# Kernel tuning notes

Measured on AMD Instinct MI355X. Metric: run time of the kernel, lower is better.

## Reference

```python
import jax, jax.numpy as jnp
import numpy as np

B = 16384; NF = 16; VOCAB = 100000; ED = 32; NNUM = 13
E = 8; T = 2; H0 = 512; H1 = 256; TH = 128
D0 = NF * ED + NNUM  # 525
EPS = 1e-5


def setup_inputs() -> dict:
    key = jax.random.key(0)
    ks = jax.random.split(key, 24)
    f32 = jnp.float32
    return {
        "categorical_x": jax.random.randint(ks[0], (B, NF), 0, VOCAB),
        "numerical_x": jax.random.normal(ks[1], (B, NNUM), f32),
        "epoch": 5,  # >= M -> MoE (not if_neuron) branch
        "emb_table": jax.random.normal(ks[2], (NF * VOCAB, ED), f32) * 0.05,
        "W0": jax.random.normal(ks[3], (E, D0, H0), f32) * 0.05,
        "b0": jnp.zeros((E, H0), f32),
        "bn0_gamma": 1.0 + 0.1 * jax.random.normal(ks[4], (H0,), f32),
        "bn0_beta": 0.1 * jax.random.normal(ks[5], (H0,), f32),
        "bn0_mean": 0.1 * jax.random.normal(ks[6], (H0,), f32),
        "bn0_var": 0.5 + jax.random.uniform(ks[7], (H0,), f32),
        "W1": jax.random.normal(ks[8], (E, H0, H1), f32) * 0.05,
        "b1": jnp.zeros((E, H1), f32),
        "bn1_gamma": 1.0 + 0.1 * jax.random.normal(ks[9], (H1,), f32),
        "bn1_beta": 0.1 * jax.random.normal(ks[10], (H1,), f32),
        "bn1_mean": 0.1 * jax.random.normal(ks[11], (H1,), f32),
        "bn1_var": 0.5 + jax.random.uniform(ks[12], (H1,), f32),
        "Wg": jax.random.normal(ks[13], (T, D0, E), f32) * 0.05,
        "bg": jnp.zeros((T, E), f32),
        "Wt1": jax.random.normal(ks[14], (T, H1, TH), f32) * 0.05,
        "bt1": jnp.zeros((T, TH), f32),
        "tbn_gamma": 1.0 + 0.1 * jax.random.normal(ks[15], (T, TH), f32),
        "tbn_beta": 0.1 * jax.random.normal(ks[16], (T, TH), f32),
        "tbn_mean": 0.1 * jax.random.normal(ks[17], (T, TH), f32),
        "tbn_var": 0.5 + jax.random.uniform(ks[18], (T, TH), f32),
        "Wt2": jax.random.normal(ks[19], (T, TH, 1), f32) * 0.05,
        "bt2": jnp.zeros((T, 1), f32),
    }


def reference(categorical_x, numerical_x, epoch, emb_table,
              W0, b0, bn0_gamma, bn0_beta, bn0_mean, bn0_var,
              W1, b1, bn1_gamma, bn1_beta, bn1_mean, bn1_var,
              Wg, bg, Wt1, bt1, tbn_gamma, tbn_beta, tbn_mean, tbn_var,
              Wt2, bt2):
    # --- embedding + concat ---
    offsets = jnp.arange(NF, dtype=categorical_x.dtype) * VOCAB
    emb = emb_table[categorical_x + offsets[None, :]].reshape(B, NF * ED)
    x = jnp.concatenate([emb, numerical_x], axis=1)  # [B, D0]

    def bn(h, g, b, m, v):  # eval-mode BatchNorm1d, params shared across experts
        return (h - m) * jax.lax.rsqrt(v + EPS) * g + b

    # --- per-expert layer 0: grouped GEMM + shared BN/ReLU (Dropout eval=id) ---
    h = jnp.einsum('bd,edk->ebk', x, W0) + b0[:, None, :]          # [E,B,H0]
    h = jax.nn.relu(bn(h, bn0_gamma, bn0_beta, bn0_mean, bn0_var))
    # --- per-expert layer 1 ---
    h = jnp.einsum('ebd,edk->ebk', h, W1) + b1[:, None, :]          # [E,B,H1]
    h = jax.nn.relu(bn(h, bn1_gamma, bn1_beta, bn1_mean, bn1_var))

    expert_output = jnp.transpose(h, (1, 0, 2))                     # [B,E,H1]
    # --- per-task softmax gates over the raw input, bmm combine ---
    gates = jax.nn.softmax(jnp.einsum('bd,tde->tbe', x, Wg) + bg[:, None, :], axis=-1)  # [T,B,E]
    fea = jnp.einsum('tbe,bek->tbk', gates, expert_output)          # [T,B,H1]

    # --- per-task tower MLP: Linear -> BN -> ReLU -> Linear, sigmoid ---
    t = jnp.einsum('tbk,tkh->tbh', fea, Wt1) + bt1[:, None, :]      # [T,B,TH]
    t = (t - tbn_mean[:, None, :]) * jax.lax.rsqrt(tbn_var[:, None, :] + EPS)
    t = jax.nn.relu(t * tbn_gamma[:, None, :] + tbn_beta[:, None, :])
    out = (jnp.einsum('tbh,tho->tbo', t, Wt2) + bt2[:, None, :])[..., 0]  # [T,B]
    return jax.nn.sigmoid(out)
```

## Files before the change

### kernel.cpp

```cpp
#include <hip/hip_runtime.h>
#include <hip/hip_bf16.h>

#define B_ 16384
#define NF_ 16
#define VOCAB_ 100000
#define ED_ 32
#define NNUM_ 13
#define E_ 8
#define T_ 2
#define H0_ 512
#define H1_ 256
#define TH_ 128
#define D0_ 525
#define K0P 576

#define BM 128
#define BN 128
#define BKK 64

typedef __bf16 bf16x8 __attribute__((ext_vector_type(8)));
typedef float  f32x4  __attribute__((ext_vector_type(4)));
typedef int    i32x4  __attribute__((ext_vector_type(4)));

typedef __attribute__((address_space(3))) void lds_void;
typedef __attribute__((address_space(1))) const void gbl_void;

__device__ __forceinline__ void load_lds16(const void* g, void* l) {
  __builtin_amdgcn_global_load_lds((gbl_void*)g, (lds_void*)l, 16, 0, 0);
}

__global__ __launch_bounds__(192) void k_embed(const int* __restrict__ cat,
                                               const float* __restrict__ num,
                                               const float* __restrict__ emb,
                                               __hip_bfloat16* __restrict__ x) {
  int b = blockIdx.x;
  int t = threadIdx.x;
  const int* crow = cat + b * NF_;
#pragma unroll
  for (int i = 0; i < 3; ++i) {
    int d = t + i * 192;
    float v;
    if (d < 512) {
      int f = d >> 5, c = d & 31;
      v = emb[((long long)(f * VOCAB_ + crow[f])) * ED_ + c];
    } else if (d < D0_) {
      v = num[b * NNUM_ + (d - 512)];
    } else {
      v = 0.f;
    }
    x[(long long)b * K0P + d] = __float2bfloat16(v);
  }
}

__global__ __launch_bounds__(256) void k_wprep(const float* __restrict__ W,
                                               __hip_bfloat16* __restrict__ Wp,
                                               int K, int N, int KP) {
  __shared__ float tile[64][65];
  int k0 = blockIdx.x * 64, n0 = blockIdx.y * 64, e = blockIdx.z;
  int tx = threadIdx.x & 63, ty = threadIdx.x >> 6;
  for (int r = ty; r < 64; r += 4) {
    int k = k0 + r;
    tile[r][tx] = (k < K) ? W[((long long)e * K + k) * N + n0 + tx] : 0.f;
  }
  __syncthreads();
  for (int r = ty; r < 64; r += 4) {
    int n = n0 + r;
    Wp[((long long)e * N + n) * KP + k0 + tx] = __float2bfloat16(tile[tx][r]);
  }
}

__global__ void k_prep_small(const float* b0, const float* g0, const float* be0,
                             const float* m0, const float* v0,
                             const float* b1, const float* g1, const float* be1,
                             const float* m1, const float* v1,
                             const float* bt1, const float* tg, const float* tb,
                             const float* tm, const float* tv,
                             float* scale0, float* ebias0, float* scale1, float* ebias1,
                             float* tscale, float* tbias) {
  int i = blockIdx.x * 256 + threadIdx.x;
  if (i < H0_) scale0[i] = g0[i] * rsqrtf(v0[i] + 1e-5f);
  if (i < H1_) scale1[i] = g1[i] * rsqrtf(v1[i] + 1e-5f);
  if (i < T_ * TH_) {
    float s = tg[i] * rsqrtf(tv[i] + 1e-5f);
    tscale[i] = s;
    tbias[i] = (bt1[i] - tm[i]) * s + tb[i];
  }
  if (i < E_ * H0_) {
    int n = i & (H0_ - 1);
    float s = g0[n] * rsqrtf(v0[n] + 1e-5f);
    ebias0[i] = (b0[i] - m0[n]) * s + be0[n];
  }
  if (i < E_ * H1_) {
    int n = i & (H1_ - 1);
    float s = g1[n] * rsqrtf(v1[n] + 1e-5f);
    ebias1[i] = (b1[i] - m1[n]) * s + be1[n];
  }
}

__global__ __launch_bounds__(256) void k_gates(const __hip_bfloat16* __restrict__ x,
                                               const float* __restrict__ Wg,
                                               const float* __restrict__ bg,
                                               float* __restrict__ gates) {
  int gidx = blockIdx.x * 256 + threadIdx.x;
  int b = gidx >> 4, te = gidx & 15;
  int t = te >> 3, e = te & 7;
  const __hip_bfloat16* xr = x + (long long)b * K0P;
  const float* wg = Wg + ((long long)t * D0_) * E_ + e;
  float acc = bg[t * E_ + e];
  int k = 0;
  for (; k + 8 <= D0_; k += 8) {
    bf16x8 xv = *reinterpret_cast<const bf16x8*>(xr + k);
#pragma unroll
    for (int j = 0; j < 8; ++j)
      acc += (float)xv[j] * wg[(long long)(k + j) * E_];
  }
  for (; k < D0_; ++k) acc += __bfloat162float(xr[k]) * wg[(long long)k * E_];
  float mx = acc;
#pragma unroll
  for (int o = 1; o < 8; o <<= 1) mx = fmaxf(mx, __shfl_xor(mx, o));
  float p = __expf(acc - mx);
  float s = p;
#pragma unroll
  for (int o = 1; o < 8; o <<= 1) s += __shfl_xor(s, o);
  gates[((long long)t * B_ + b) * E_ + e] = p / s;
}

__global__ __launch_bounds__(256) void k_gemm(
    const __hip_bfloat16* __restrict__ Aall, long long strideAe, int lda,
    const __hip_bfloat16* __restrict__ Ball, long long strideBe, int ldb,
    __hip_bfloat16* __restrict__ Call, long long strideCe, int N,
    const float* __restrict__ scale, const float* __restrict__ ebias, int strideEb,
    int K) {
  __shared__ __align__(16) char As[BM * 128];
  __shared__ __align__(16) char Bs[BN * 128];

  const int e = blockIdx.z;
  const char* A = reinterpret_cast<const char*>(Aall + (long long)e * strideAe +
                                                (long long)blockIdx.x * BM * lda);
  const char* Bw = reinterpret_cast<const char*>(Ball + (long long)e * strideBe +
                                                 (long long)blockIdx.y * BN * ldb);
  const int ldab = lda * 2, ldbb = ldb * 2;

  const int tid = threadIdx.x;
  const int lane = tid & 63;
  const int wid = tid >> 6;
  const int wr = wid >> 1, wc = wid & 1;

  const int baserow = wid * 32 + (lane >> 3);
  const int swz = ((lane & 7) << 4) ^ ((lane >> 3) << 4);

  f32x4 acc[4][4];
#pragma unroll
  for (int m = 0; m < 4; ++m)
#pragma unroll
    for (int n = 0; n < 4; ++n) acc[m][n] = (f32x4){0.f, 0.f, 0.f, 0.f};

  const int nk = K / BKK;
  for (int ks = 0; ks < nk; ++ks) {
    const int kb0 = ks * 128;
#pragma unroll
    for (int i = 0; i < 4; ++i) {
      const int row = baserow + i * 8;
      load_lds16(A + (long long)row * ldab + kb0 + swz, As + (wid * 4 + i) * 1024);
      load_lds16(Bw + (long long)row * ldbb + kb0 + swz, Bs + (wid * 4 + i) * 1024);
    }
    __syncthreads();
#pragma unroll
    for (int kk = 0; kk < 2; ++kk) {
      bf16x8 af[4], bfr[4];
      int kb = kk * 64 + (lane >> 4) * 16;
#pragma unroll
      for (int m = 0; m < 4; ++m) {
        int row = wr * 64 + m * 16 + (lane & 15);
        af[m] = *reinterpret_cast<const bf16x8*>(As + row * 128 + (kb ^ ((row & 7) << 4)));
      }
#pragma unroll
      for (int n = 0; n < 4; ++n) {
        int row = wc * 64 + n * 16 + (lane & 15);
        bfr[n] = *reinterpret_cast<const bf16x8*>(Bs + row * 128 + (kb ^ ((row & 7) << 4)));
      }
#pragma unroll
      for (int m = 0; m < 4; ++m)
#pragma unroll
        for (int n = 0; n < 4; ++n)
          acc[m][n] = __builtin_amdgcn_mfma_f32_16x16x32_bf16(af[m], bfr[n], acc[m][n], 0, 0, 0);
    }
    __syncthreads();
  }

  __hip_bfloat16* C = Call + (long long)e * strideCe;
  const float* eb = ebias + e * strideEb;
  const int m0 = blockIdx.x * BM, n0 = blockIdx.y * BN;
#pragma unroll
  for (int n = 0; n < 4; ++n) {
    int col = n0 + wc * 64 + n * 16 + (lane & 15);
    float s = scale[col];
    float bb = eb[col];
#pragma unroll
    for (int m = 0; m < 4; ++m) {
      int rowb = m0 + wr * 64 + m * 16 + (lane >> 4) * 4;
#pragma unroll
      for (int i = 0; i < 4; ++i) {
        float v = fmaxf(acc[m][n][i] * s + bb, 0.f);
        C[(long long)(rowb + i) * N + col] = __float2bfloat16(v);
      }
    }
  }
}

__global__ __launch_bounds__(256) void k_tower(
    const __hip_bfloat16* __restrict__ h1, const float* __restrict__ gates,
    const float* __restrict__ Wt1, const float* __restrict__ Wt2,
    const float* __restrict__ bt2, const float* __restrict__ tscale,
    const float* __restrict__ tbias, float* __restrict__ out) {
  __shared__ __align__(16) char Ws[TH_ * 512];
  const int tid = threadIdx.x;
  const int lane = tid & 63, wv = tid >> 6;

  const int row = blockIdx.x * 64 + wv * 16 + (lane & 15);
  const int g4 = lane >> 4;

  float gt0[8], gt1[8];
  {
    const float* gp0 = gates + (long long)row * E_;
    const float* gp1 = gates + ((long long)B_ + row) * E_;
#pragma unroll
    for (int j = 0; j < 8; ++j) { gt0[j] = gp0[j]; gt1[j] = gp1[j]; }
  }

  float fa0[8][8], fa1[8][8];
#pragma unroll
  for (int c = 0; c < 8; ++c)
#pragma unroll
    for (int j = 0; j < 8; ++j) { fa0[c][j] = 0.f; fa1[c][j] = 0.f; }

#pragma unroll
  for (int ee = 0; ee < 8; ++ee) {
    const char* hp = reinterpret_cast<const char*>(h1) +
                     (((long long)ee * B_ + row) * H1_ + g4 * 8) * 2;
    float ga = gt0[ee], gb = gt1[ee];
#pragma unroll
    for (int c = 0; c < 8; ++c) {
      bf16x8 hv = *reinterpret_cast<const bf16x8*>(hp + c * 64);
#pragma unroll
      for (int j = 0; j < 8; ++j) {
        float v = (float)hv[j];
        fa0[c][j] += ga * v;
        fa1[c][j] += gb * v;
      }
    }
  }
  bf16x8 af0[8], af1[8];
#pragma unroll
  for (int c = 0; c < 8; ++c)
#pragma unroll
    for (int j = 0; j < 8; ++j) {
      af0[c][j] = (__bf16)fa0[c][j];
      af1[c][j] = (__bf16)fa1[c][j];
    }

#pragma unroll
  for (int t = 0; t < T_; ++t) {
    if (t) __syncthreads();
    for (int it = 0; it < 16; ++it) {
      int idx = it * 256 + tid;
      int h = idx & 127, kc = idx >> 7;
      bf16x8 v;
#pragma unroll
      for (int j = 0; j < 8; ++j)
        v[j] = (__bf16)Wt1[((long long)t * H1_ + kc * 8 + j) * TH_ + h];
      int byt = h * 512 + ((kc * 16) ^ ((h & 7) << 4));
      *reinterpret_cast<bf16x8*>(Ws + byt) = v;
    }
    __syncthreads();

    f32x4 acc[8];
#pragma unroll
    for (int n = 0; n < 8; ++n) acc[n] = (f32x4){0.f, 0.f, 0.f, 0.f};
#pragma unroll
    for (int c = 0; c < 8; ++c) {
      int kb = c * 64 + g4 * 16;
#pragma unroll
      for (int n = 0; n < 8; ++n) {
        int hrow = n * 16 + (lane & 15);
        bf16x8 bv = *reinterpret_cast<const bf16x8*>(Ws + hrow * 512 + (kb ^ ((hrow & 7) << 4)));
        acc[n] = __builtin_amdgcn_mfma_f32_16x16x32_bf16(t ? af1[c] : af0[c], bv, acc[n], 0, 0, 0);
      }
    }

    float part[4] = {0.f, 0.f, 0.f, 0.f};
#pragma unroll
    for (int n = 0; n < 8; ++n) {
      int col = n * 16 + (lane & 15);
      float s = tscale[t * TH_ + col], bb = tbias[t * TH_ + col], w2 = Wt2[t * TH_ + col];
#pragma unroll
      for (int i = 0; i < 4; ++i)
        part[i] += fmaxf(acc[n][i] * s + bb, 0.f) * w2;
    }
#pragma unroll
    for (int o = 1; o < 16; o <<= 1) {
#pragma unroll
      for (int i = 0; i < 4; ++i) part[i] += __shfl_xor(part[i], o);
    }
    if ((lane & 15) == 0) {
      int rbase = blockIdx.x * 64 + wv * 16 + g4 * 4;
      float b2 = bt2[t];
#pragma unroll
      for (int i = 0; i < 4; ++i) {
        float z = part[i] + b2;
        out[(long long)t * B_ + rbase + i] = 1.f / (1.f + __expf(-z));
      }
    }
  }
}

extern "C" void kernel_launch(void* const* d_in, const int* in_sizes, int n_in,
                              void* d_out, int out_size, void* d_ws, size_t ws_size,
                              hipStream_t stream) {
  const int*   cat = (const int*)d_in[0];
  const float* num = (const float*)d_in[1];
  const float* emb = (const float*)d_in[3];
  const float* W0  = (const float*)d_in[4];
  const float* b0  = (const float*)d_in[5];
  const float* g0  = (const float*)d_in[6];
  const float* be0 = (const float*)d_in[7];
  const float* m0  = (const float*)d_in[8];
  const float* v0  = (const float*)d_in[9];
  const float* W1  = (const float*)d_in[10];
  const float* b1  = (const float*)d_in[11];
  const float* g1  = (const float*)d_in[12];
  const float* be1 = (const float*)d_in[13];
  const float* m1  = (const float*)d_in[14];
  const float* v1  = (const float*)d_in[15];
  const float* Wg  = (const float*)d_in[16];
  const float* bg  = (const float*)d_in[17];
  const float* Wt1 = (const float*)d_in[18];
  const float* bt1 = (const float*)d_in[19];
  const float* tg  = (const float*)d_in[20];
  const float* tb  = (const float*)d_in[21];
  const float* tm  = (const float*)d_in[22];
  const float* tv  = (const float*)d_in[23];
  const float* Wt2 = (const float*)d_in[24];
  const float* bt2 = (const float*)d_in[25];
  float* out = (float*)d_out;

  char* ws = (char*)d_ws;
  if (ws_size < 228094976ULL) return;

  __hip_bfloat16* x_bf = (__hip_bfloat16*)(ws + 0ULL);
  __hip_bfloat16* W0p  = (__hip_bfloat16*)(ws + 18874368ULL);
  __hip_bfloat16* W1p  = (__hip_bfloat16*)(ws + 23592960ULL);
  float* gates   = (float*)(ws + 25690112ULL);
  float* scale0  = (float*)(ws + 26738688ULL);
  float* ebias0  = (float*)(ws + 26740736ULL);
  float* scale1  = (float*)(ws + 26757120ULL);
  float* ebias1  = (float*)(ws + 26758144ULL);
  float* tscale  = (float*)(ws + 26766336ULL);
  float* tbias   = (float*)(ws + 26767360ULL);
  __hip_bfloat16* h0 = (__hip_bfloat16*)(ws + 26768384ULL);
  __hip_bfloat16* h1 = (__hip_bfloat16*)(ws + 160986112ULL);

  k_wprep<<<dim3(K0P / 64, H0_ / 64, E_), 256, 0, stream>>>(W0, W0p, D0_, H0_, K0P);
  k_wprep<<<dim3(H0_ / 64, H1_ / 64, E_), 256, 0, stream>>>(W1, W1p, H0_, H1_, H0_);
  k_prep_small<<<16, 256, 0, stream>>>(b0, g0, be0, m0, v0, b1, g1, be1, m1, v1,
                                       bt1, tg, tb, tm, tv,
                                       scale0, ebias0, scale1, ebias1, tscale, tbias);
  k_embed<<<B_, 192, 0, stream>>>(cat, num, emb, x_bf);
  k_gates<<<B_ * 16 / 256, 256, 0, stream>>>(x_bf, Wg, bg, gates);
  k_gemm<<<dim3(B_ / BM, H0_ / BN, E_), 256, 0, stream>>>(
      x_bf, 0LL, K0P, W0p, (long long)H0_ * K0P, K0P,
      h0, (long long)B_ * H0_, H0_, scale0, ebias0, H0_, K0P);
  k_gemm<<<dim3(B_ / BM, H1_ / BN, E_), 256, 0, stream>>>(
      h0, (long long)B_ * H0_, H0_, W1p, (long long)H1_ * H0_, H0_,
      h1, (long long)B_ * H1_, H1_, scale1, ebias1, H1_, H0_);
  k_tower<<<dim3(B_ / 64), 256, 0, stream>>>(h1, gates, Wt1, Wt2, bt2,
                                             tscale, tbias, out);
}
```

Baseline: 312.9 us.

## Enlarge GEMM tiles to 256x256 with double-buffered LDS prefetch

The grouped expert GEMM moves from 128x128 tiles with 256 threads to 256x256 tiles with 512 threads (8 waves, each computing 128x64). The LDS staging is double-buffered so the next K tile's global-to-LDS loads are issued before computing the current one, with explicit vmcnt waits and raw barriers. It also raises MFMA wave priority with s_setprio. The larger tiles raise data reuse and cut global traffic, but they use 128KB of LDS and 128 accumulator registers per thread. This may limit occupancy and leaves fewer blocks for the second GEMM (N=256 gives one column tile).

```diff
diff --git a/kernel.cpp b/kernel.cpp
--- a/kernel.cpp
+++ b/kernel.cpp
@@ -14,9 +14,8 @@
 #define D0_ 525
 #define K0P 576
 
-#define BM 128
-#define BN 128
-#define BKK 64
+#define GBM 256
+#define GBN 256
 
 typedef __bf16 bf16x8 __attribute__((ext_vector_type(8)));
 typedef float  f32x4  __attribute__((ext_vector_type(4)));
@@ -25,7 +24,7 @@
 typedef __attribute__((address_space(3))) void lds_void;
 typedef __attribute__((address_space(1))) const void gbl_void;
 
-__device__ __forceinline__ void load_lds16(const void* g, void* l) {
+__device__ __forceinline__ void load_lds16f(const void* g, void* l) {
   __builtin_amdgcn_global_load_lds((gbl_void*)g, (lds_void*)l, 16, 0, 0);
 }
 
@@ -125,80 +124,113 @@
   gates[((long long)t * B_ + b) * E_ + e] = p / s;
 }
 
-__global__ __launch_bounds__(256) void k_gemm(
+__global__ __launch_bounds__(512, 2) void k_gemm(
     const __hip_bfloat16* __restrict__ Aall, long long strideAe, int lda,
     const __hip_bfloat16* __restrict__ Ball, long long strideBe, int ldb,
     __hip_bfloat16* __restrict__ Call, long long strideCe, int N,
     const float* __restrict__ scale, const float* __restrict__ ebias, int strideEb,
     int K) {
-  __shared__ __align__(16) char As[BM * 128];
-  __shared__ __align__(16) char Bs[BN * 128];
+  __shared__ __align__(16) char As[2][32768];
+  __shared__ __align__(16) char Bs[2][32768];
 
   const int e = blockIdx.z;
   const char* A = reinterpret_cast<const char*>(Aall + (long long)e * strideAe +
-                                                (long long)blockIdx.x * BM * lda);
+                                                (long long)blockIdx.x * GBM * lda);
   const char* Bw = reinterpret_cast<const char*>(Ball + (long long)e * strideBe +
-                                                 (long long)blockIdx.y * BN * ldb);
+                                                 (long long)blockIdx.y * GBN * ldb);
   const int ldab = lda * 2, ldbb = ldb * 2;
 
   const int tid = threadIdx.x;
   const int lane = tid & 63;
   const int wid = tid >> 6;
-  const int wr = wid >> 1, wc = wid & 1;
-
-  const int baserow = wid * 32 + (lane >> 3);
-  const int swz = ((lane & 7) << 4) ^ ((lane >> 3) << 4);
-
-  f32x4 acc[4][4];
-#pragma unroll
-  for (int m = 0; m < 4; ++m)
+  const int wr = wid >> 2, wc = wid & 3;
+
+  const int stg_row = tid >> 3;
+  const int swz = ((tid & 7) << 4) ^ ((stg_row & 7) << 4);
+
+  f32x4 acc[8][4];
+#pragma unroll
+  for (int m = 0; m < 8; ++m)
 #pragma unroll
     for (int n = 0; n < 4; ++n) acc[m][n] = (f32x4){0.f, 0.f, 0.f, 0.f};
 
-  const int nk = K / BKK;
-  for (int ks = 0; ks < nk; ++ks) {
-    const int kb0 = ks * 128;
-#pragma unroll
-    for (int i = 0; i < 4; ++i) {
-      const int row = baserow + i * 8;
-      load_lds16(A + (long long)row * ldab + kb0 + swz, As + (wid * 4 + i) * 1024);
-      load_lds16(Bw + (long long)row * ldbb + kb0 + swz, Bs + (wid * 4 + i) * 1024);
-    }
-    __syncthreads();
-#pragma unroll
-    for (int kk = 0; kk < 2; ++kk) {
-      bf16x8 af[4], bfr[4];
-      int kb = kk * 64 + (lane >> 4) * 16;
-#pragma unroll
-      for (int m = 0; m < 4; ++m) {
-        int row = wr * 64 + m * 16 + (lane & 15);
-        af[m] = *reinterpret_cast<const bf16x8*>(As + row * 128 + (kb ^ ((row & 7) << 4)));
+  const int nk = K / 64;
+
+#define STAGE_TILE(kt_, s_)                                                     \
+  do {                                                                          \
+    const long long kb0_ = (long long)(kt_) * 128;                              \
+    char* adst_ = As[(s_)] + tid * 16;                                          \
+    char* bdst_ = Bs[(s_)] + tid * 16;                                          \
+    _Pragma("unroll")                                                           \
+    for (int i_ = 0; i_ < 4; ++i_) {                                            \
+      const int row_ = stg_row + i_ * 64;                                       \
+      load_lds16f(A + (long long)row_ * ldab + kb0_ + swz, adst_ + i_ * 8192);  \
+      load_lds16f(Bw + (long long)row_ * ldbb + kb0_ + swz, bdst_ + i_ * 8192); \
+    }                                                                           \
+  } while (0)
+
+  STAGE_TILE(0, 0);
+
+  for (int kt = 0; kt < nk; ++kt) {
+    const int cur = kt & 1;
+    if (kt + 1 < nk) {
+      STAGE_TILE(kt + 1, cur ^ 1);
+      asm volatile("s_waitcnt vmcnt(8)" ::: "memory");
+    } else {
+      asm volatile("s_waitcnt vmcnt(0)" ::: "memory");
+    }
+    __builtin_amdgcn_s_barrier();
+
+    const char* Ab = As[cur];
+    const char* Bb = Bs[cur];
+#pragma unroll
+    for (int mh = 0; mh < 2; ++mh)
+#pragma unroll
+      for (int nh = 0; nh < 2; ++nh) {
+        bf16x8 af[2][4], bq[2][2];
+#pragma unroll
+        for (int kk = 0; kk < 2; ++kk) {
+          const int kb = kk * 64 + (lane >> 4) * 16;
+#pragma unroll
+          for (int m = 0; m < 4; ++m) {
+            const int row = wr * 128 + (mh * 4 + m) * 16 + (lane & 15);
+            af[kk][m] = *reinterpret_cast<const bf16x8*>(
+                Ab + row * 128 + (kb ^ ((row & 7) << 4)));
+          }
+#pragma unroll
+          for (int n = 0; n < 2; ++n) {
+            const int row = wc * 64 + (nh * 2 + n) * 16 + (lane & 15);
+            bq[kk][n] = *reinterpret_cast<const bf16x8*>(
+                Bb + row * 128 + (kb ^ ((row & 7) << 4)));
+          }
+        }
+        __builtin_amdgcn_s_setprio(1);
+#pragma unroll
+        for (int kk = 0; kk < 2; ++kk)
+#pragma unroll
+          for (int m = 0; m < 4; ++m)
+#pragma unroll
+            for (int n = 0; n < 2; ++n)
+              acc[mh * 4 + m][nh * 2 + n] = __builtin_amdgcn_mfma_f32_16x16x32_bf16(
+                  af[kk][m], bq[kk][n], acc[mh * 4 + m][nh * 2 + n], 0, 0, 0);
+        __builtin_amdgcn_s_setprio(0);
       }
-#pragma unroll
-      for (int n = 0; n < 4; ++n) {
-        int row = wc * 64 + n * 16 + (lane & 15);
-        bfr[n] = *reinterpret_cast<const bf16x8*>(Bs + row * 128 + (kb ^ ((row & 7) << 4)));
-      }
-#pragma unroll
-      for (int m = 0; m < 4; ++m)
-#pragma unroll
-        for (int n = 0; n < 4; ++n)
-          acc[m][n] = __builtin_amdgcn_mfma_f32_16x16x32_bf16(af[m], bfr[n], acc[m][n], 0, 0, 0);
-    }
-    __syncthreads();
-  }
+    asm volatile("" ::: "memory");
+    __builtin_amdgcn_s_barrier();
+  }
+#undef STAGE_TILE
 
   __hip_bfloat16* C = Call + (long long)e * strideCe;
   const float* eb = ebias + e * strideEb;
-  const int m0 = blockIdx.x * BM, n0 = blockIdx.y * BN;
+  const int m0 = blockIdx.x * GBM, n0 = blockIdx.y * GBN;
 #pragma unroll
   for (int n = 0; n < 4; ++n) {
     int col = n0 + wc * 64 + n * 16 + (lane & 15);
     float s = scale[col];
     float bb = eb[col];
 #pragma unroll
-    for (int m = 0; m < 4; ++m) {
-      int rowb = m0 + wr * 64 + m * 16 + (lane >> 4) * 4;
+    for (int m = 0; m < 8; ++m) {
+      int rowb = m0 + wr * 128 + m * 16 + (lane >> 4) * 4;
 #pragma unroll
       for (int i = 0; i < 4; ++i) {
         float v = fmaxf(acc[m][n][i] * s + bb, 0.f);
@@ -367,10 +399,10 @@
                                        scale0, ebias0, scale1, ebias1, tscale, tbias);
   k_embed<<<B_, 192, 0, stream>>>(cat, num, emb, x_bf);
   k_gates<<<B_ * 16 / 256, 256, 0, stream>>>(x_bf, Wg, bg, gates);
-  k_gemm<<<dim3(B_ / BM, H0_ / BN, E_), 256, 0, stream>>>(
+  k_gemm<<<dim3(B_ / GBM, H0_ / GBN, E_), 512, 0, stream>>>(
       x_bf, 0LL, K0P, W0p, (long long)H0_ * K0P, K0P,
       h0, (long long)B_ * H0_, H0_, scale0, ebias0, H0_, K0P);
-  k_gemm<<<dim3(B_ / BM, H1_ / BN, E_), 256, 0, stream>>>(
+  k_gemm<<<dim3(B_ / GBM, H1_ / GBN, E_), 512, 0, stream>>>(
       h0, (long long)B_ * H0_, H0_, W1p, (long long)H1_ * H0_, H0_,
       h1, (long long)B_ * H1_, H1_, scale1, ebias1, H1_, H0_);
   k_tower<<<dim3(B_ / 64), 256, 0, stream>>>(h1, gates, Wt1, Wt2, bt2,
```

New measurement: 318.4 us. Within noise of the previous version (+1.7%).

## Rewrite expert GEMM as 256x256 double-buffered ping-pong pipeline with 8 waves

Applied to the files above, without the earlier changes.

Replaces the 128x128 single-buffered GEMM with a 256x256 tile per 512-thread block. Each operand is split into halves and double-buffered in LDS, and async global-to-LDS loads are interleaved with quadrant MFMA phases behind explicit barriers and setprio. The K padding is raised from 576 to 640 so the K loop runs an even number of 64-wide steps, which adds some zero-padded work in layer 0. The aim is to hide load latency and raise arithmetic intensity, at the cost of 128KB of LDS per block, more registers and lower occupancy.

```diff
diff --git a/kernel.cpp b/kernel.cpp
--- a/kernel.cpp
+++ b/kernel.cpp
@@ -12,24 +12,32 @@
 #define H1_ 256
 #define TH_ 128
 #define D0_ 525
-#define K0P 576
-
-#define BM 128
-#define BN 128
-#define BKK 64
+#define K0P 640
 
 typedef __bf16 bf16x8 __attribute__((ext_vector_type(8)));
 typedef float  f32x4  __attribute__((ext_vector_type(4)));
-typedef int    i32x4  __attribute__((ext_vector_type(4)));
 
 typedef __attribute__((address_space(3))) void lds_void;
 typedef __attribute__((address_space(1))) const void gbl_void;
 
-__device__ __forceinline__ void load_lds16(const void* g, void* l) {
+__device__ __forceinline__ void load_lds16f(const void* g, void* l) {
   __builtin_amdgcn_global_load_lds((gbl_void*)g, (lds_void*)l, 16, 0, 0);
 }
 
-__global__ __launch_bounds__(192) void k_embed(const int* __restrict__ cat,
+#define BARX                                        \
+  do {                                              \
+    asm volatile("" ::: "memory");                  \
+    __builtin_amdgcn_s_barrier();                   \
+    __builtin_amdgcn_sched_barrier(0);              \
+    asm volatile("" ::: "memory");                  \
+  } while (0)
+#define LGKM0                                       \
+  do {                                              \
+    asm volatile("s_waitcnt lgkmcnt(0)" ::: "memory"); \
+    __builtin_amdgcn_sched_barrier(0);              \
+  } while (0)
+
+__global__ __launch_bounds__(256) void k_embed(const int* __restrict__ cat,
                                                const float* __restrict__ num,
                                                const float* __restrict__ emb,
                                                __hip_bfloat16* __restrict__ x) {
@@ -38,7 +46,8 @@
   const int* crow = cat + b * NF_;
 #pragma unroll
   for (int i = 0; i < 3; ++i) {
-    int d = t + i * 192;
+    int d = t + i * 256;
+    if (d >= K0P) continue;
     float v;
     if (d < 512) {
       int f = d >> 5, c = d & 31;
@@ -125,87 +134,159 @@
   gates[((long long)t * B_ + b) * E_ + e] = p / s;
 }
 
-__global__ __launch_bounds__(256) void k_gemm(
+__global__ __launch_bounds__(512, 2) void k_gemm(
     const __hip_bfloat16* __restrict__ Aall, long long strideAe, int lda,
     const __hip_bfloat16* __restrict__ Ball, long long strideBe, int ldb,
     __hip_bfloat16* __restrict__ Call, long long strideCe, int N,
     const float* __restrict__ scale, const float* __restrict__ ebias, int strideEb,
     int K) {
-  __shared__ __align__(16) char As[BM * 128];
-  __shared__ __align__(16) char Bs[BN * 128];
+  __shared__ __align__(16) char As[2][2][16384];
+  __shared__ __align__(16) char Bs[2][2][16384];
 
   const int e = blockIdx.z;
   const char* A = reinterpret_cast<const char*>(Aall + (long long)e * strideAe +
-                                                (long long)blockIdx.x * BM * lda);
+                                                (long long)blockIdx.x * 256 * lda);
   const char* Bw = reinterpret_cast<const char*>(Ball + (long long)e * strideBe +
-                                                 (long long)blockIdx.y * BN * ldb);
+                                                 (long long)blockIdx.y * 256 * ldb);
   const int ldab = lda * 2, ldbb = ldb * 2;
 
   const int tid = threadIdx.x;
   const int lane = tid & 63;
   const int wid = tid >> 6;
-  const int wr = wid >> 1, wc = wid & 1;
-
-  const int baserow = wid * 32 + (lane >> 3);
-  const int swz = ((lane & 7) << 4) ^ ((lane >> 3) << 4);
-
-  f32x4 acc[4][4];
-#pragma unroll
-  for (int m = 0; m < 4; ++m)
-#pragma unroll
-    for (int n = 0; n < 4; ++n) acc[m][n] = (f32x4){0.f, 0.f, 0.f, 0.f};
-
-  const int nk = K / BKK;
-  for (int ks = 0; ks < nk; ++ks) {
-    const int kb0 = ks * 128;
-#pragma unroll
-    for (int i = 0; i < 4; ++i) {
-      const int row = baserow + i * 8;
-      load_lds16(A + (long long)row * ldab + kb0 + swz, As + (wid * 4 + i) * 1024);
-      load_lds16(Bw + (long long)row * ldbb + kb0 + swz, Bs + (wid * 4 + i) * 1024);
-    }
-    __syncthreads();
+  const int wq_r = wid >> 2, wq_c = wid & 3;
+
+  const int srow = tid >> 3;
+  const int swz = ((tid & 7) << 4) ^ ((srow & 7) << 4);
+
+  auto STG_A = [&](int kt, int half, int slot) {
+#pragma unroll
+    for (int j = 0; j < 2; ++j) {
+      const int lrow = srow + j * 64;
+      load_lds16f(A + (long long)(half * 128 + lrow) * ldab + kt * 128 + swz,
+                  &As[slot][half][j * 8192 + tid * 16]);
+    }
+  };
+  auto STG_B = [&](int kt, int half, int slot) {
+#pragma unroll
+    for (int j = 0; j < 2; ++j) {
+      const int lrow = srow + j * 64;
+      load_lds16f(Bw + (long long)(half * 128 + lrow) * ldbb + kt * 128 + swz,
+                  &Bs[slot][half][j * 8192 + tid * 16]);
+    }
+  };
+
+  bf16x8 af[2][4], bq[2][2];
+  auto LDA = [&](int slot, int half) {
 #pragma unroll
     for (int kk = 0; kk < 2; ++kk) {
-      bf16x8 af[4], bfr[4];
-      int kb = kk * 64 + (lane >> 4) * 16;
+      const int kb = kk * 64 + (lane >> 4) * 16;
 #pragma unroll
       for (int m = 0; m < 4; ++m) {
-        int row = wr * 64 + m * 16 + (lane & 15);
-        af[m] = *reinterpret_cast<const bf16x8*>(As + row * 128 + (kb ^ ((row & 7) << 4)));
-      }
-#pragma unroll
-      for (int n = 0; n < 4; ++n) {
-        int row = wc * 64 + n * 16 + (lane & 15);
-        bfr[n] = *reinterpret_cast<const bf16x8*>(Bs + row * 128 + (kb ^ ((row & 7) << 4)));
-      }
+        const int lrow = wq_r * 64 + m * 16 + (lane & 15);
+        af[kk][m] = *reinterpret_cast<const bf16x8*>(
+            &As[slot][half][lrow * 128 + (kb ^ ((lane & 7) << 4))]);
+      }
+    }
+  };
+  auto LDB = [&](int slot, int half) {
+#pragma unroll
+    for (int kk = 0; kk < 2; ++kk) {
+      const int kb = kk * 64 + (lane >> 4) * 16;
+#pragma unroll
+      for (int n = 0; n < 2; ++n) {
+        const int lrow = wq_c * 32 + n * 16 + (lane & 15);
+        bq[kk][n] = *reinterpret_cast<const bf16x8*>(
+            &Bs[slot][half][lrow * 128 + (kb ^ ((lane & 7) << 4))]);
+      }
+    }
+  };
+
+  f32x4 acc[2][2][4][2];
+#pragma unroll
+  for (int a = 0; a < 2; ++a)
+#pragma unroll
+    for (int b = 0; b < 2; ++b)
 #pragma unroll
       for (int m = 0; m < 4; ++m)
 #pragma unroll
-        for (int n = 0; n < 4; ++n)
-          acc[m][n] = __builtin_amdgcn_mfma_f32_16x16x32_bf16(af[m], bfr[n], acc[m][n], 0, 0, 0);
-    }
-    __syncthreads();
-  }
+        for (int n = 0; n < 2; ++n) acc[a][b][m][n] = (f32x4){0.f, 0.f, 0.f, 0.f};
+
+#define MMQ(QM, QN)                                                            \
+  do {                                                                         \
+    __builtin_amdgcn_s_setprio(1);                                             \
+    _Pragma("unroll") for (int kk = 0; kk < 2; ++kk)                           \
+        _Pragma("unroll") for (int m = 0; m < 4; ++m)                          \
+            _Pragma("unroll") for (int n = 0; n < 2; ++n)                      \
+                acc[QM][QN][m][n] = __builtin_amdgcn_mfma_f32_16x16x32_bf16(   \
+                    af[kk][m], bq[kk][n], acc[QM][QN][m][n], 0, 0, 0);         \
+    __builtin_amdgcn_s_setprio(0);                                             \
+  } while (0)
+
+  const int nk = K / 64;
+  const int nj = nk / 2;
+
+  STG_A(0, 0, 0); STG_A(0, 1, 0); STG_B(0, 0, 0); STG_B(0, 1, 0);
+  if (nk > 1) { STG_A(1, 0, 1); STG_B(1, 1, 1); }
+  asm volatile("s_waitcnt vmcnt(4)" ::: "memory");
+  BARX;
+
+  for (int j = 0; j < nj; ++j) {
+    const int t1 = 2 * j + 1, t2 = 2 * j + 2, t3 = 2 * j + 3;
+    const bool more = (t2 < nk);
+    LDA(0, 0); LDB(0, 0);
+    STG_A(t1, 1, 1);
+    BARX; LGKM0; MMQ(0, 0); BARX;
+    LDB(0, 1);
+    STG_B(t1, 0, 1);
+    BARX; LGKM0; MMQ(0, 1); BARX;
+    LDA(0, 1);
+    if (more) STG_A(t2, 0, 0);
+    BARX; LGKM0; MMQ(1, 1); BARX;
+    LDB(0, 0);
+    if (more) STG_B(t2, 1, 0);
+    BARX; LGKM0; MMQ(1, 0);
+    if (more) { asm volatile("s_waitcnt vmcnt(4)" ::: "memory"); }
+    else      { asm volatile("s_waitcnt vmcnt(0)" ::: "memory"); }
+    BARX;
+    LDA(1, 0); LDB(1, 0);
+    if (more) STG_A(t2, 1, 0);
+    BARX; LGKM0; MMQ(0, 0); BARX;
+    LDB(1, 1);
+    if (more) STG_B(t2, 0, 0);
+    BARX; LGKM0; MMQ(0, 1); BARX;
+    LDA(1, 1);
+    if (more) STG_A(t3, 0, 1);
+    BARX; LGKM0; MMQ(1, 1); BARX;
+    LDB(1, 0);
+    if (more) STG_B(t3, 1, 1);
+    BARX; LGKM0; MMQ(1, 0);
+    if (more) { asm volatile("s_waitcnt vmcnt(4)" ::: "memory"); }
+    BARX;
+  }
+#undef MMQ
 
   __hip_bfloat16* C = Call + (long long)e * strideCe;
   const float* eb = ebias + e * strideEb;
-  const int m0 = blockIdx.x * BM, n0 = blockIdx.y * BN;
-#pragma unroll
-  for (int n = 0; n < 4; ++n) {
-    int col = n0 + wc * 64 + n * 16 + (lane & 15);
-    float s = scale[col];
-    float bb = eb[col];
-#pragma unroll
-    for (int m = 0; m < 4; ++m) {
-      int rowb = m0 + wr * 64 + m * 16 + (lane >> 4) * 4;
-#pragma unroll
-      for (int i = 0; i < 4; ++i) {
-        float v = fmaxf(acc[m][n][i] * s + bb, 0.f);
-        C[(long long)(rowb + i) * N + col] = __float2bfloat16(v);
-      }
-    }
-  }
+  const int m0 = blockIdx.x * 256, n0 = blockIdx.y * 256;
+#pragma unroll
+  for (int Qm = 0; Qm < 2; ++Qm)
+#pragma unroll
+    for (int Qn = 0; Qn < 2; ++Qn)
+#pragma unroll
+      for (int n = 0; n < 2; ++n) {
+        const int col = n0 + Qn * 128 + wq_c * 32 + n * 16 + (lane & 15);
+        const float s = scale[col];
+        const float bb = eb[col];
+#pragma unroll
+        for (int m = 0; m < 4; ++m) {
+          const int rowb = m0 + Qm * 128 + wq_r * 64 + m * 16 + (lane >> 4) * 4;
+#pragma unroll
+          for (int i = 0; i < 4; ++i) {
+            float v = fmaxf(acc[Qm][Qn][m][n][i] * s + bb, 0.f);
+            C[(long long)(rowb + i) * N + col] = __float2bfloat16(v);
+          }
+        }
+      }
 }
 
 __global__ __launch_bounds__(256) void k_tower(
@@ -345,32 +426,32 @@
   float* out = (float*)d_out;
 
   char* ws = (char*)d_ws;
-  if (ws_size < 228094976ULL) return;
+  if (ws_size < 230719488ULL) return;
 
   __hip_bfloat16* x_bf = (__hip_bfloat16*)(ws + 0ULL);
-  __hip_bfloat16* W0p  = (__hip_bfloat16*)(ws + 18874368ULL);
-  __hip_bfloat16* W1p  = (__hip_bfloat16*)(ws + 23592960ULL);
-  float* gates   = (float*)(ws + 25690112ULL);
-  float* scale0  = (float*)(ws + 26738688ULL);
-  float* ebias0  = (float*)(ws + 26740736ULL);
-  float* scale1  = (float*)(ws + 26757120ULL);
-  float* ebias1  = (float*)(ws + 26758144ULL);
-  float* tscale  = (float*)(ws + 26766336ULL);
-  float* tbias   = (float*)(ws + 26767360ULL);
-  __hip_bfloat16* h0 = (__hip_bfloat16*)(ws + 26768384ULL);
-  __hip_bfloat16* h1 = (__hip_bfloat16*)(ws + 160986112ULL);
+  __hip_bfloat16* W0p  = (__hip_bfloat16*)(ws + 20971520ULL);
+  __hip_bfloat16* W1p  = (__hip_bfloat16*)(ws + 26214400ULL);
+  float* gates   = (float*)(ws + 28311552ULL);
+  float* scale0  = (float*)(ws + 29360128ULL);
+  float* ebias0  = (float*)(ws + 29362176ULL);
+  float* scale1  = (float*)(ws + 29378560ULL);
+  float* ebias1  = (float*)(ws + 29379584ULL);
+  float* tscale  = (float*)(ws + 29387776ULL);
+  float* tbias   = (float*)(ws + 29388800ULL);
+  __hip_bfloat16* h0 = (__hip_bfloat16*)(ws + 29392896ULL);
+  __hip_bfloat16* h1 = (__hip_bfloat16*)(ws + 163610624ULL);
 
   k_wprep<<<dim3(K0P / 64, H0_ / 64, E_), 256, 0, stream>>>(W0, W0p, D0_, H0_, K0P);
   k_wprep<<<dim3(H0_ / 64, H1_ / 64, E_), 256, 0, stream>>>(W1, W1p, H0_, H1_, H0_);
   k_prep_small<<<16, 256, 0, stream>>>(b0, g0, be0, m0, v0, b1, g1, be1, m1, v1,
                                        bt1, tg, tb, tm, tv,
                                        scale0, ebias0, scale1, ebias1, tscale, tbias);
-  k_embed<<<B_, 192, 0, stream>>>(cat, num, emb, x_bf);
+  k_embed<<<B_, 256, 0, stream>>>(cat, num, emb, x_bf);
   k_gates<<<B_ * 16 / 256, 256, 0, stream>>>(x_bf, Wg, bg, gates);
-  k_gemm<<<dim3(B_ / BM, H0_ / BN, E_), 256, 0, stream>>>(
+  k_gemm<<<dim3(B_ / 256, H0_ / 256, E_), 512, 0, stream>>>(
       x_bf, 0LL, K0P, W0p, (long long)H0_ * K0P, K0P,
       h0, (long long)B_ * H0_, H0_, scale0, ebias0, H0_, K0P);
-  k_gemm<<<dim3(B_ / BM, H1_ / BN, E_), 256, 0, stream>>>(
+  k_gemm<<<dim3(B_ / 256, H1_ / 256, E_), 512, 0, stream>>>(
       h0, (long long)B_ * H0_, H0_, W1p, (long long)H1_ * H0_, H0_,
       h1, (long long)B_ * H1_, H1_, scale1, ebias1, H1_, H0_);
   k_tower<<<dim3(B_ / 64), 256, 0, stream>>>(h1, gates, Wt1, Wt2, bt2,
```

New measurement: 294.9 us. 1.06x faster.
